# Performance work log

Hardware: AMD Instinct MI355X
Metric: run time of the kernel (lower is better)

The kernel has to match this reference:

```python
import jax, jax.numpy as jnp
import numpy as np

TEMPERATURE = 1.0

N = 20000  # = subsample, so the random-subsample branch is not taken


def setup_inputs() -> dict:
    key = jax.random.key(0)
    k1, k2 = jax.random.split(key)
    logits = jax.random.normal(k1, (N,), dtype=jnp.float32)
    targets = jax.random.uniform(k2, (N,), dtype=jnp.float32)  # relevance in [0,1]
    return {"logits": logits, "targets": targets}


def reference(logits, targets):
    s = logits.reshape(-1)
    y = targets.reshape(-1)
    n = s.shape[0]
    t = jnp.asarray(TEMPERATURE, dtype=s.dtype)

    # diff[i, j] = s[j] - s[i]; approx rank of item j = 1 + sum_i sigmoid((s[j]-s[i])/T)
    diff = s[None, :] - s[:, None]                     # [n, n]
    approx_rank = jax.nn.sigmoid(diff / t).sum(axis=0) + 1.0

    discount = 1.0 / jnp.log2(approx_rank + 1.0)
    dcg = jnp.sum(y * discount)

    ideal_rank = jnp.arange(1, n + 1, dtype=s.dtype)
    ideal_discount = 1.0 / jnp.log2(ideal_rank + 1.0)
    sorted_y = jnp.sort(y)[::-1]                        # descending
    idcg = jnp.sum(sorted_y * ideal_discount)

    ndcg = dcg / (idcg + 1e-8)
    loss = 1.0 - ndcg
    # early-return guard: if total relevance < 1, loss is 0
    return jnp.where(jnp.sum(y) < 1.0, jnp.zeros((), dtype=s.dtype), loss)
```

## Files before the change

### kernel.cpp

```cpp
#include <hip/hip_runtime.h>


#define LOG2E 1.442695040888963387f
#define M_NODES 64
#define XHALF 8.0
#define NB 2048
#define PI_D 3.14159265358979323846
#define BT 1024
#define LDS_N 20480
#define MAXN 131072

#if __has_builtin(__builtin_amdgcn_exp2f)
#define EXP2(x) __builtin_amdgcn_exp2f(x)
#else
#define EXP2(x) exp2f(x)
#endif

#if __has_builtin(__builtin_amdgcn_rcpf)
#define RCP(x) __builtin_amdgcn_rcpf(x)
#else
#define RCP(x) (1.0f / (x))
#endif

__device__ double g_acc[3] = {0.0, 0.0, 0.0};
__device__ int g_done = 0;
__device__ float2 g_nodes[M_NODES];
__device__ int g_prefix[NB + 1];
__device__ float g_ybkt[MAXN];

__device__ __forceinline__ int bucket_of(float y) {
  int b = (int)(y * (float)NB);
  return b < 0 ? 0 : (b > NB - 1 ? NB - 1 : b);
}

__global__ __launch_bounds__(BT) void produce_kernel(
    const float* __restrict__ s, const float* __restrict__ y, int n) {
  const int tid = threadIdx.x;
  const int blk = blockIdx.x;
  const int lane = tid & 63;

  __shared__ int hist[NB];
  __shared__ float ybkt_l[LDS_N];
  __shared__ int wrep[16];
  __shared__ double wsum[16];

  if (blk == 0) {
    for (int b = tid; b < NB; b += BT) hist[b] = 0;
    __syncthreads();

    const float4* y4 = (const float4*)y;
    const int n4 = n >> 2;
    for (int i = tid; i < n4; i += BT) {
      const float4 v = y4[i];
      atomicAdd(&hist[bucket_of(v.x)], 1);
      atomicAdd(&hist[bucket_of(v.y)], 1);
      atomicAdd(&hist[bucket_of(v.z)], 1);
      atomicAdd(&hist[bucket_of(v.w)], 1);
    }
    for (int i = (n4 << 2) + tid; i < n; i += BT)
      atomicAdd(&hist[bucket_of(y[i])], 1);
    __syncthreads();

    const int base = tid * 2;
    const int l0 = hist[base], l1 = hist[base + 1];
    const int sum2 = l0 + l1;
    int v = sum2;
#pragma unroll
    for (int d = 1; d < 64; d <<= 1) {
      const int t = __shfl_up(v, d);
      if (lane >= d) v += t;
    }
    if (lane == 63) wrep[tid >> 6] = v;
    __syncthreads();
    if (tid < 16) {
      int wv = wrep[tid];
#pragma unroll
      for (int d = 1; d < 16; d <<= 1) {
        const int t = __shfl_up(wv, d);
        if (tid >= d) wv += t;
      }
      wrep[tid] = wv;
    }
    __syncthreads();
    const int wbase = (tid >> 6) ? wrep[(tid >> 6) - 1] : 0;
    const int incl = wbase + v;
    const int run = incl - sum2;
    g_prefix[base] = run;
    g_prefix[base + 1] = run + l0;
    if (tid == BT - 1) g_prefix[NB] = incl;
    hist[base] = run;
    hist[base + 1] = run + l0;
    __syncthreads();

    if (n <= LDS_N) {
      for (int i = tid; i < n4; i += BT) {
        const float4 v4 = y4[i];
        ybkt_l[atomicAdd(&hist[bucket_of(v4.x)], 1)] = v4.x;
        ybkt_l[atomicAdd(&hist[bucket_of(v4.y)], 1)] = v4.y;
        ybkt_l[atomicAdd(&hist[bucket_of(v4.z)], 1)] = v4.z;
        ybkt_l[atomicAdd(&hist[bucket_of(v4.w)], 1)] = v4.w;
      }
      for (int i = (n4 << 2) + tid; i < n; i += BT) {
        const float yv = y[i];
        ybkt_l[atomicAdd(&hist[bucket_of(yv)], 1)] = yv;
      }
      __syncthreads();
      const int nv = (n + 3) >> 2;
      float4* gb4 = (float4*)g_ybkt;
      const float4* lb4 = (const float4*)ybkt_l;
      for (int i = tid; i < nv; i += BT) gb4[i] = lb4[i];
    } else {
      for (int i = tid; i < n4; i += BT) {
        const float4 v4 = y4[i];
        g_ybkt[atomicAdd(&hist[bucket_of(v4.x)], 1)] = v4.x;
        g_ybkt[atomicAdd(&hist[bucket_of(v4.y)], 1)] = v4.y;
        g_ybkt[atomicAdd(&hist[bucket_of(v4.z)], 1)] = v4.z;
        g_ybkt[atomicAdd(&hist[bucket_of(v4.w)], 1)] = v4.w;
      }
      for (int i = (n4 << 2) + tid; i < n; i += BT) {
        const float yv = y[i];
        g_ybkt[atomicAdd(&hist[bucket_of(yv)], 1)] = yv;
      }
    }
  } else {
    const int k = blk - 1;
    const float xk =
        (float)(XHALF * cos(PI_D * (double)k / (double)(M_NODES - 1)));
    double F = 0.0;
    const float4* s4 = (const float4*)s;
    const int n4 = n >> 2;
    for (int i = tid; i < n4; i += BT) {
      const float4 v = s4[i];
      float t = RCP(1.0f + EXP2((v.x - xk) * LOG2E));
      t += RCP(1.0f + EXP2((v.y - xk) * LOG2E));
      t += RCP(1.0f + EXP2((v.z - xk) * LOG2E));
      t += RCP(1.0f + EXP2((v.w - xk) * LOG2E));
      F += (double)t;
    }
    for (int i = (n4 << 2) + tid; i < n; i += BT)
      F += (double)RCP(1.0f + EXP2((s[i] - xk) * LOG2E));
    for (int off = 32; off > 0; off >>= 1) F += __shfl_down(F, off);
    if (lane == 0) wsum[tid >> 6] = F;
    __syncthreads();
    if (tid == 0) {
      double t = 0.0;
#pragma unroll
      for (int w = 0; w < 16; ++w) t += wsum[w];
      g_nodes[k] = make_float2(xk, (float)t);
    }
  }
}

__global__ __launch_bounds__(256) void consume_kernel(
    const float* __restrict__ s, const float* __restrict__ y,
    float* __restrict__ out, int n, int nblocks) {
  __shared__ float2 nd[M_NODES];
  __shared__ double wsum[12];
  const int tid = threadIdx.x;
  if (tid < M_NODES) nd[tid] = g_nodes[tid];
  __syncthreads();

  const int j = blockIdx.x * 256 + tid;
  double dc = 0.0, ic = 0.0, ys = 0.0;
  if (j < n) {
    const float x = s[j];
    const float yj = y[j];
    double num = 0.0, den = 0.0;
    int hit = -1;
#pragma unroll
    for (int k = 0; k < M_NODES; ++k) {
      const float d = x - nd[k].x;
      float w = (k & 1) ? -1.0f : 1.0f;
      if (k == 0 || k == M_NODES - 1) w *= 0.5f;
      if (d == 0.0f) {
        hit = k;
      } else {
        const float iv = w * RCP(d);
        num += (double)iv * (double)nd[k].y;
        den += (double)iv;
      }
    }
    const double F = (hit >= 0) ? (double)nd[hit].y : (num / den);

    const int b = bucket_of(yj);
    const int s0 = g_prefix[b];
    const int s1 = g_prefix[b + 1];
    int cnt = n - s1;
    for (int t = s0; t < s1; ++t) cnt += (g_ybkt[t] > yj);

    dc = (double)yj / log2(F + 2.0);
    ic = (double)yj / log2((double)cnt + 2.0);
    ys = (double)yj;
  }
  for (int off = 32; off > 0; off >>= 1) {
    dc += __shfl_down(dc, off);
    ic += __shfl_down(ic, off);
    ys += __shfl_down(ys, off);
  }
  const int wv = tid >> 6;
  if ((tid & 63) == 0) {
    wsum[wv] = dc;
    wsum[wv + 4] = ic;
    wsum[wv + 8] = ys;
  }
  __syncthreads();
  if (tid == 0) {
    atomicAdd(&g_acc[0], wsum[0] + wsum[1] + wsum[2] + wsum[3]);
    atomicAdd(&g_acc[1], wsum[4] + wsum[5] + wsum[6] + wsum[7]);
    atomicAdd(&g_acc[2], wsum[8] + wsum[9] + wsum[10] + wsum[11]);
    __threadfence();
    const int old = atomicAdd(&g_done, 1);
    if (old == nblocks - 1) {
      const double dcg = atomicAdd(&g_acc[0], 0.0);
      const double idcg = atomicAdd(&g_acc[1], 0.0);
      const double ysum = atomicAdd(&g_acc[2], 0.0);
      const double loss = 1.0 - dcg / (idcg + 1e-8);
      out[0] = (ysum < 1.0) ? 0.0f : (float)loss;
      g_acc[0] = 0.0;
      g_acc[1] = 0.0;
      g_acc[2] = 0.0;
      g_done = 0;
      __threadfence();
    }
  }
}

extern "C" void kernel_launch(void* const* d_in, const int* in_sizes, int n_in,
                              void* d_out, int out_size, void* d_ws,
                              size_t ws_size, hipStream_t stream) {
  const float* s = (const float*)d_in[0];
  const float* y = (const float*)d_in[1];
  const int n = in_sizes[0];
  (void)d_ws;
  (void)ws_size;

  const int nb = (n + 255) / 256;
  produce_kernel<<<M_NODES + 1, BT, 0, stream>>>(s, y, n);
  consume_kernel<<<nb, 256, 0, stream>>>(s, y, (float*)d_out, n, nb);
}
```

Measured before the change: 73.91 us.

## Fully sort relevance buckets in producer so consumer reads ideal rank directly

After bucketing targets by value, each producer thread insertion-sorts its two buckets, giving a fully ascending sorted array. The consumer then computes the IDCG term from the sorted position (rank n-j) instead of scanning each item's bucket to count larger values. This removes the per-item global bucket scan but adds a serial insertion sort inside the single histogram block, which lengthens the producer's critical path. Ties are handled by position rather than by a strict-greater count, which matches a true sort.

```diff
diff --git a/kernel.cpp b/kernel.cpp
--- a/kernel.cpp
+++ b/kernel.cpp
@@ -7,6 +7,7 @@
 #define NB 2048
 #define PI_D 3.14159265358979323846
 #define BT 1024
+#define CT 256
 #define LDS_N 20480
 #define MAXN 131072
 
@@ -40,6 +41,7 @@
   const int lane = tid & 63;
 
   __shared__ int hist[NB];
+  __shared__ int sbeg[NB];
   __shared__ float ybkt_l[LDS_N];
   __shared__ int wrep[16];
   __shared__ double wsum[16];
@@ -88,6 +90,8 @@
     g_prefix[base] = run;
     g_prefix[base + 1] = run + l0;
     if (tid == BT - 1) g_prefix[NB] = incl;
+    sbeg[base] = run;
+    sbeg[base + 1] = run + l0;
     hist[base] = run;
     hist[base + 1] = run + l0;
     __syncthreads();
@@ -105,6 +109,23 @@
         ybkt_l[atomicAdd(&hist[bucket_of(yv)], 1)] = yv;
       }
       __syncthreads();
+
+#pragma unroll
+      for (int q = 0; q < 2; ++q) {
+        const int b = base + q;
+        const int lo = sbeg[b], hi = hist[b];
+        for (int i = lo + 1; i < hi; ++i) {
+          const float vv = ybkt_l[i];
+          int k = i - 1;
+          while (k >= lo && ybkt_l[k] > vv) {
+            ybkt_l[k + 1] = ybkt_l[k];
+            --k;
+          }
+          ybkt_l[k + 1] = vv;
+        }
+      }
+      __syncthreads();
+
       const int nv = (n + 3) >> 2;
       float4* gb4 = (float4*)g_ybkt;
       const float4* lb4 = (const float4*)ybkt_l;
@@ -120,6 +141,21 @@
       for (int i = (n4 << 2) + tid; i < n; i += BT) {
         const float yv = y[i];
         g_ybkt[atomicAdd(&hist[bucket_of(yv)], 1)] = yv;
+      }
+      __syncthreads();
+#pragma unroll
+      for (int q = 0; q < 2; ++q) {
+        const int b = base + q;
+        const int lo = g_prefix[b], hi = hist[b];
+        for (int i = lo + 1; i < hi; ++i) {
+          const float vv = g_ybkt[i];
+          int k = i - 1;
+          while (k >= lo && g_ybkt[k] > vv) {
+            g_ybkt[k + 1] = g_ybkt[k];
+            --k;
+          }
+          g_ybkt[k + 1] = vv;
+        }
       }
     }
   } else {
@@ -151,7 +187,7 @@
   }
 }
 
-__global__ __launch_bounds__(256) void consume_kernel(
+__global__ __launch_bounds__(CT) void consume_kernel(
     const float* __restrict__ s, const float* __restrict__ y,
     float* __restrict__ out, int n, int nblocks) {
   __shared__ float2 nd[M_NODES];
@@ -160,11 +196,12 @@
   if (tid < M_NODES) nd[tid] = g_nodes[tid];
   __syncthreads();
 
-  const int j = blockIdx.x * 256 + tid;
+  const int j = blockIdx.x * CT + tid;
   double dc = 0.0, ic = 0.0, ys = 0.0;
   if (j < n) {
     const float x = s[j];
     const float yj = y[j];
+
     double num = 0.0, den = 0.0;
     int hit = -1;
 #pragma unroll
@@ -181,15 +218,11 @@
       }
     }
     const double F = (hit >= 0) ? (double)nd[hit].y : (num / den);
-
-    const int b = bucket_of(yj);
-    const int s0 = g_prefix[b];
-    const int s1 = g_prefix[b + 1];
-    int cnt = n - s1;
-    for (int t = s0; t < s1; ++t) cnt += (g_ybkt[t] > yj);
-
     dc = (double)yj / log2(F + 2.0);
-    ic = (double)yj / log2((double)cnt + 2.0);
+
+    const float yv = g_ybkt[j];
+    ic = (double)yv / log2((double)(n - j) + 1.0);
+
     ys = (double)yj;
   }
   for (int off = 32; off > 0; off >>= 1) {
@@ -234,7 +267,7 @@
   (void)d_ws;
   (void)ws_size;
 
-  const int nb = (n + 255) / 256;
+  const int nb = (n + CT - 1) / CT;
   produce_kernel<<<M_NODES + 1, BT, 0, stream>>>(s, y, n);
-  consume_kernel<<<nb, 256, 0, stream>>>(s, y, (float*)d_out, n, nb);
-}
+  consume_kernel<<<nb, CT, 0, stream>>>(s, y, (float*)d_out, n, nb);
+}
```

Result: slower. 100.3 us (+35.7%).
